# Performance work log

Hardware: AMD Instinct MI355X
Metric: run time of the kernel (lower is better)

## Reference

```python
import jax, jax.numpy as jnp
import numpy as np

INPUT_SZ = 4096
HIDDEN_SZ = 4096


def setup_inputs() -> dict:
    key = jax.random.key(0)
    ks = jax.random.split(key, 19)
    s_in = 1.0 / np.sqrt(INPUT_SZ)
    s_h = 1.0 / np.sqrt(HIDDEN_SZ)
    d = {"x_t": jax.random.normal(ks[0], (INPUT_SZ,), dtype=jnp.float32)}
    names_i = ["W_ii", "W_if", "W_ig", "W_io"]
    names_h = ["W_hi", "W_hf", "W_hg", "W_ho"]
    names_b = ["b_ii", "b_if", "b_ig", "b_io", "b_hi", "b_hf", "b_hg", "b_ho"]
    k = 1
    for n in names_i:
        d[n] = jax.random.normal(ks[k], (INPUT_SZ, HIDDEN_SZ), dtype=jnp.float32) * s_in
        k += 1
    for n in names_h:
        d[n] = jax.random.normal(ks[k], (HIDDEN_SZ, HIDDEN_SZ), dtype=jnp.float32) * s_h
        k += 1
    for n in names_b:
        d[n] = jax.random.normal(ks[k], (HIDDEN_SZ,), dtype=jnp.float32) * s_h
        k += 1
    # initial states (module defaults to zeros)
    d["h_t"] = jnp.zeros((HIDDEN_SZ,), dtype=jnp.float32)
    d["c_t"] = jnp.zeros((HIDDEN_SZ,), dtype=jnp.float32)
    return d


def reference(x_t, W_ii, W_if, W_ig, W_io, W_hi, W_hf, W_hg, W_ho,
              b_ii, b_if, b_ig, b_io, b_hi, b_hf, b_hg, b_ho, h_t, c_t):
    # Fuse the 8 GEMVs into 2 by concatenating gate weights along hidden axis.
    Wi = jnp.concatenate([W_ii, W_if, W_ig, W_io], axis=1)  # [in, 4H]
    Wh = jnp.concatenate([W_hi, W_hf, W_hg, W_ho], axis=1)  # [H, 4H]
    b = jnp.concatenate([b_ii + b_hi, b_if + b_hf, b_ig + b_hg, b_io + b_ho])
    gates = x_t @ Wi + h_t @ Wh + b  # [4H]
    H = h_t.shape[0]
    i_t = jax.nn.sigmoid(gates[0:H])
    f_t = jax.nn.sigmoid(gates[H:2 * H])
    g_t = jnp.tanh(gates[2 * H:3 * H])
    o_t = jax.nn.sigmoid(gates[3 * H:4 * H])
    c_new = f_t * c_t + i_t * g_t
    h_new = o_t * jnp.tanh(c_new)
    return h_new
```

## Files before the change

kernel.cpp:

```cpp
#include <hip/hip_runtime.h>
#include <math.h>

#define HSZ 4096
#define CHUNK 64
#define COLS_PER_BLOCK 1024
#define NBLK_PER_MAT 256

struct WPtrs { const float* W[8]; };
struct BPtrs { const float* b[8]; };

__global__ __launch_bounds__(256) void lstm_gemv_kernel(
        WPtrs wp, const float* __restrict__ x, const float* __restrict__ hv,
        float* __restrict__ gates) {
    int mat = blockIdx.x >> 8;
    int rem = blockIdx.x & (NBLK_PER_MAT - 1);
    int ct  = rem & 3;
    int kc  = rem >> 2;
    const float* __restrict__ W = wp.W[mat];
    const float* __restrict__ v = (mat < 4) ? x : hv;

    __shared__ float vs[CHUNK];
    __shared__ int nz;
    int tid = threadIdx.x;
    if (tid == 0) nz = 0;
    __syncthreads();
    if (tid < CHUNK) {
        float val = v[kc * CHUNK + tid];
        vs[tid] = val;
        if (__any(val != 0.0f) && tid == 0) nz = 1;
    }
    __syncthreads();
    if (!nz) return;

    int col = ct * COLS_PER_BLOCK + tid * 4;
    const float* Wp = W + (size_t)kc * CHUNK * HSZ + col;
    float4 acc = make_float4(0.f, 0.f, 0.f, 0.f);
#pragma unroll
    for (int kk = 0; kk < CHUNK; kk += 8) {
        float4 w[8];
#pragma unroll
        for (int u = 0; u < 8; ++u)
            w[u] = *(const float4*)(Wp + (size_t)(kk + u) * HSZ);
#pragma unroll
        for (int u = 0; u < 8; ++u) {
            float xv = vs[kk + u];
            acc.x = fmaf(xv, w[u].x, acc.x);
            acc.y = fmaf(xv, w[u].y, acc.y);
            acc.z = fmaf(xv, w[u].z, acc.z);
            acc.w = fmaf(xv, w[u].w, acc.w);
        }
    }
    float* g = gates + (size_t)(mat & 3) * HSZ + col;
    atomicAdd(g + 0, acc.x);
    atomicAdd(g + 1, acc.y);
    atomicAdd(g + 2, acc.z);
    atomicAdd(g + 3, acc.w);
}

__device__ __forceinline__ float sigmoidf_fast(float v) {
    return 1.0f / (1.0f + __expf(-v));
}

__global__ void lstm_final_kernel(const float* __restrict__ gates, BPtrs bp,
                                  const float* __restrict__ c,
                                  float* __restrict__ out) {
    int j = blockIdx.x * 256 + threadIdx.x;
    float ig = gates[j]           + bp.b[0][j] + bp.b[4][j];
    float fg = gates[HSZ + j]     + bp.b[1][j] + bp.b[5][j];
    float gg = gates[2 * HSZ + j] + bp.b[2][j] + bp.b[6][j];
    float og = gates[3 * HSZ + j] + bp.b[3][j] + bp.b[7][j];
    float it = sigmoidf_fast(ig);
    float ft = sigmoidf_fast(fg);
    float gt = tanhf(gg);
    float ot = sigmoidf_fast(og);
    float cn = ft * c[j] + it * gt;
    out[j] = ot * tanhf(cn);
}

extern "C" void kernel_launch(void* const* d_in, const int* in_sizes, int n_in,
                              void* d_out, int out_size, void* d_ws, size_t ws_size,
                              hipStream_t stream) {
    const float* x = (const float*)d_in[0];
    WPtrs wp;
    for (int i = 0; i < 8; ++i) wp.W[i] = (const float*)d_in[1 + i];
    BPtrs bp;
    for (int i = 0; i < 8; ++i) bp.b[i] = (const float*)d_in[9 + i];
    const float* h = (const float*)d_in[17];
    const float* c = (const float*)d_in[18];

    float* gates = (float*)d_ws;

    hipMemsetAsync(gates, 0, 4 * HSZ * sizeof(float), stream);
    lstm_gemv_kernel<<<8 * NBLK_PER_MAT, 256, 0, stream>>>(wp, x, h, gates);
    lstm_final_kernel<<<HSZ / 256, 256, 0, stream>>>(gates, bp, c, (float*)d_out);
}
```

Baseline: 414.6 us.

## Replace input-GEMV atomics with per-slab partial sums and a reduction kernel

The input-side GEMV blocks now each cover 16 rows across all 4096 columns and write their partial results to a workspace buffer instead of doing float atomics into the gate vector. A new reduction kernel sums the 256 slab partials per gate, then adds the hidden-side atomic results and both biases. The bias adds move out of the final activation kernel. This removes most of the global atomic traffic, at the cost of about 16 MB of extra partial-sum writes and reads plus one more kernel launch.

```diff
diff --git a/kernel.cpp b/kernel.cpp
--- a/kernel.cpp
+++ b/kernel.cpp
@@ -1,74 +1,118 @@
 #include <hip/hip_runtime.h>
 #include <math.h>
 
-#define HSZ 4096
-#define CHUNK 64
-#define COLS_PER_BLOCK 1024
-#define NBLK_PER_MAT 256
+#define HSZ   4096
+#define RROWS 16
+#define NSLAB 256
 
 struct WPtrs { const float* W[8]; };
 struct BPtrs { const float* b[8]; };
 
-__global__ __launch_bounds__(256) void lstm_gemv_kernel(
+__device__ __forceinline__ void fma4(float4& a, float s, float4 w) {
+    a.x = fmaf(s, w.x, a.x);
+    a.y = fmaf(s, w.y, a.y);
+    a.z = fmaf(s, w.z, a.z);
+    a.w = fmaf(s, w.w, a.w);
+}
+
+__global__ __launch_bounds__(256, 8) void lstm_gemv_kernel(
         WPtrs wp, const float* __restrict__ x, const float* __restrict__ hv,
-        float* __restrict__ gates) {
-    int mat = blockIdx.x >> 8;
-    int rem = blockIdx.x & (NBLK_PER_MAT - 1);
-    int ct  = rem & 3;
-    int kc  = rem >> 2;
-    const float* __restrict__ W = wp.W[mat];
+        float* __restrict__ px, float* __restrict__ hg) {
+    const int mat  = blockIdx.x >> 8;
+    const int slab = blockIdx.x & (NSLAB - 1);
+    const int tid  = threadIdx.x;
     const float* __restrict__ v = (mat < 4) ? x : hv;
 
-    __shared__ float vs[CHUNK];
+    __shared__ float vs[RROWS];
     __shared__ int nz;
-    int tid = threadIdx.x;
     if (tid == 0) nz = 0;
     __syncthreads();
-    if (tid < CHUNK) {
-        float val = v[kc * CHUNK + tid];
-        vs[tid] = val;
+    if (tid < 64) {
+        float val = (tid < RROWS) ? v[slab * RROWS + tid] : 0.0f;
+        if (tid < RROWS) vs[tid] = val;
         if (__any(val != 0.0f) && tid == 0) nz = 1;
     }
     __syncthreads();
-    if (!nz) return;
+    if (mat >= 4 && !nz) return;
 
-    int col = ct * COLS_PER_BLOCK + tid * 4;
-    const float* Wp = W + (size_t)kc * CHUNK * HSZ + col;
-    float4 acc = make_float4(0.f, 0.f, 0.f, 0.f);
+    const float* __restrict__ Wb = wp.W[mat] + (size_t)slab * RROWS * HSZ;
+    const int c0 = tid * 4;
+    float4 a0 = make_float4(0.f, 0.f, 0.f, 0.f), a1 = a0, a2 = a0, a3 = a0;
 #pragma unroll
-    for (int kk = 0; kk < CHUNK; kk += 8) {
-        float4 w[8];
+    for (int k = 0; k < RROWS; k += 2) {
+        const float* r0 = Wb + (size_t)k * HSZ + c0;
+        const float* r1 = r0 + HSZ;
+        float4 w00 = *(const float4*)(r0);
+        float4 w01 = *(const float4*)(r0 + 1024);
+        float4 w02 = *(const float4*)(r0 + 2048);
+        float4 w03 = *(const float4*)(r0 + 3072);
+        float4 w10 = *(const float4*)(r1);
+        float4 w11 = *(const float4*)(r1 + 1024);
+        float4 w12 = *(const float4*)(r1 + 2048);
+        float4 w13 = *(const float4*)(r1 + 3072);
+        float x0 = vs[k], x1 = vs[k + 1];
+        fma4(a0, x0, w00); fma4(a1, x0, w01); fma4(a2, x0, w02); fma4(a3, x0, w03);
+        fma4(a0, x1, w10); fma4(a1, x1, w11); fma4(a2, x1, w12); fma4(a3, x1, w13);
+    }
+    if (mat < 4) {
+        float* dst = px + ((size_t)slab * 4 + mat) * HSZ + c0;
+        *(float4*)(dst)        = a0;
+        *(float4*)(dst + 1024) = a1;
+        *(float4*)(dst + 2048) = a2;
+        *(float4*)(dst + 3072) = a3;
+    } else {
+        float* dst = hg + (size_t)(mat - 4) * HSZ + c0;
+        atomicAdd(dst + 0,    a0.x); atomicAdd(dst + 1,    a0.y);
+        atomicAdd(dst + 2,    a0.z); atomicAdd(dst + 3,    a0.w);
+        atomicAdd(dst + 1024, a1.x); atomicAdd(dst + 1025, a1.y);
+        atomicAdd(dst + 1026, a1.z); atomicAdd(dst + 1027, a1.w);
+        atomicAdd(dst + 2048, a2.x); atomicAdd(dst + 2049, a2.y);
+        atomicAdd(dst + 2050, a2.z); atomicAdd(dst + 2051, a2.w);
+        atomicAdd(dst + 3072, a3.x); atomicAdd(dst + 3073, a3.y);
+        atomicAdd(dst + 3074, a3.z); atomicAdd(dst + 3075, a3.w);
+    }
+}
+
+__global__ __launch_bounds__(256) void lstm_reduce_kernel(
+        const float* __restrict__ px, const float* __restrict__ hg,
+        BPtrs bp, float* __restrict__ gates) {
+    const int m  = blockIdx.x & 3;
+    const int j0 = (blockIdx.x >> 2) << 6;
+    const int jl = threadIdx.x & 63;
+    const int sg = threadIdx.x >> 6;
+    const float* p = px + ((size_t)(sg * 64) * 4 + m) * HSZ + j0 + jl;
+    float s0 = 0.f, s1 = 0.f, s2 = 0.f, s3 = 0.f;
 #pragma unroll
-        for (int u = 0; u < 8; ++u)
-            w[u] = *(const float4*)(Wp + (size_t)(kk + u) * HSZ);
-#pragma unroll
-        for (int u = 0; u < 8; ++u) {
-            float xv = vs[kk + u];
-            acc.x = fmaf(xv, w[u].x, acc.x);
-            acc.y = fmaf(xv, w[u].y, acc.y);
-            acc.z = fmaf(xv, w[u].z, acc.z);
-            acc.w = fmaf(xv, w[u].w, acc.w);
-        }
+    for (int i = 0; i < 64; i += 4) {
+        s0 += p[(size_t)(i + 0) * 4 * HSZ];
+        s1 += p[(size_t)(i + 1) * 4 * HSZ];
+        s2 += p[(size_t)(i + 2) * 4 * HSZ];
+        s3 += p[(size_t)(i + 3) * 4 * HSZ];
     }
-    float* g = gates + (size_t)(mat & 3) * HSZ + col;
-    atomicAdd(g + 0, acc.x);
-    atomicAdd(g + 1, acc.y);
-    atomicAdd(g + 2, acc.z);
-    atomicAdd(g + 3, acc.w);
+    __shared__ float red[4][64];
+    red[sg][jl] = (s0 + s1) + (s2 + s3);
+    __syncthreads();
+    if (threadIdx.x < 64) {
+        int j = j0 + threadIdx.x;
+        float t = red[0][threadIdx.x] + red[1][threadIdx.x]
+                + red[2][threadIdx.x] + red[3][threadIdx.x];
+        t += hg[m * HSZ + j] + bp.b[m][j] + bp.b[m + 4][j];
+        gates[m * HSZ + j] = t;
+    }
 }
 
 __device__ __forceinline__ float sigmoidf_fast(float v) {
     return 1.0f / (1.0f + __expf(-v));
 }
 
-__global__ void lstm_final_kernel(const float* __restrict__ gates, BPtrs bp,
+__global__ void lstm_final_kernel(const float* __restrict__ gates,
                                   const float* __restrict__ c,
                                   float* __restrict__ out) {
     int j = blockIdx.x * 256 + threadIdx.x;
-    float ig = gates[j]           + bp.b[0][j] + bp.b[4][j];
-    float fg = gates[HSZ + j]     + bp.b[1][j] + bp.b[5][j];
-    float gg = gates[2 * HSZ + j] + bp.b[2][j] + bp.b[6][j];
-    float og = gates[3 * HSZ + j] + bp.b[3][j] + bp.b[7][j];
+    float ig = gates[j];
+    float fg = gates[HSZ + j];
+    float gg = gates[2 * HSZ + j];
+    float og = gates[3 * HSZ + j];
     float it = sigmoidf_fast(ig);
     float ft = sigmoidf_fast(fg);
     float gt = tanhf(gg);
@@ -88,9 +132,12 @@
     const float* h = (const float*)d_in[17];
     const float* c = (const float*)d_in[18];
 
-    float* gates = (float*)d_ws;
+    float* px    = (float*)d_ws;
+    float* hg    = px + (size_t)NSLAB * 4 * HSZ;
+    float* gates = hg + 4 * HSZ;
 
-    hipMemsetAsync(gates, 0, 4 * HSZ * sizeof(float), stream);
-    lstm_gemv_kernel<<<8 * NBLK_PER_MAT, 256, 0, stream>>>(wp, x, h, gates);
-    lstm_final_kernel<<<HSZ / 256, 256, 0, stream>>>(gates, bp, c, (float*)d_out);
+    hipMemsetAsync(hg, 0, 4 * HSZ * sizeof(float), stream);
+    lstm_gemv_kernel<<<8 * NSLAB, 256, 0, stream>>>(wp, x, h, px, hg);
+    lstm_reduce_kernel<<<NSLAB, 256, 0, stream>>>(px, hg, bp, gates);
+    lstm_final_kernel<<<HSZ / 256, 256, 0, stream>>>(gates, c, (float*)d_out);
 }
```

Measured after the change: 420.4 us. No clear change (+1.4%).
